# Optimization experiments

Measured on AMD Instinct MI355X. Metric: run time of the kernel, lower is better.

## Reference

```python
import jax, jax.numpy as jnp
import numpy as np

D_MODEL = 2048
NUM_EXPERTS = 128
TOP_K = 8
NORM_P = 2.0  # normalize_expert_weights


def setup_inputs() -> dict:
    key = jax.random.key(0)
    k1, k2 = jax.random.split(key)
    x = jax.random.normal(k1, (4, 4096, D_MODEL), dtype=jnp.float32)
    # router weight ~ trunc_normal(std=0.02); plain normal*0.02 is fine for a numeric baseline
    weight = jax.random.normal(k2, (NUM_EXPERTS, D_MODEL), dtype=jnp.float32) * 0.02
    score_bias = jnp.zeros((NUM_EXPERTS,), dtype=jnp.float32)
    return {"x": x, "weight": weight, "score_bias": score_bias}


def reference(x, weight, score_bias):
    # Flatten tokens: (B, S, D) -> (N, D); router always runs in fp32 (x.float())
    B, S, D = x.shape
    xf = x.reshape(B * S, D).astype(jnp.float32)
    # get_expert_logits: F.linear(x, weight.view(E, D)) -> (N, E)
    logits = jnp.einsum("nd,ed->ne", xf, weight.astype(jnp.float32))
    # softmax gating
    scores = jax.nn.softmax(logits, axis=-1)
    # bias-adjusted top-k (bias only affects selection, not the returned weights)
    biased = scores + score_bias[None, :]
    _, expert_indices = jax.lax.top_k(biased, TOP_K)          # (N, top_k)
    expert_weights = jnp.take_along_axis(scores, expert_indices, axis=-1)
    # normalize_expert_weights = 2.0 -> divide by L2 norm across top_k
    norm = jnp.linalg.norm(expert_weights, ord=NORM_P, axis=-1, keepdims=True)
    expert_weights = expert_weights / norm
    return expert_weights, expert_indices
```

## Files before the change

kernel.cpp:

```cpp
#include <hip/hip_runtime.h>
#include <math.h>


#define NE      128
#define TOKT    64
#define KC      32
#define DMODEL  2048
#define NT      (DMODEL / KC)
#define CHUNK_SH (3 * NE * KC)

typedef __attribute__((ext_vector_type(8))) short short8;
typedef __attribute__((ext_vector_type(4))) short s16x4;
typedef __attribute__((ext_vector_type(4))) float f32x4;

union S4u { short s[4]; s16x4 v; };

__device__ __forceinline__ void split3(float f, S4u& hi, S4u& mi, S4u& lo, int j) {
  const unsigned u0 = __float_as_uint(f);
  const float hif = __uint_as_float(u0 & 0xFFFF0000u);
  const float r1 = f - hif;
  const unsigned u1 = __float_as_uint(r1);
  const float mif = __uint_as_float(u1 & 0xFFFF0000u);
  const float r2 = r1 - mif;
  hi.s[j] = (short)(u0 >> 16);
  mi.s[j] = (short)(u1 >> 16);
  lo.s[j] = (short)(__float_as_uint(r2) >> 16);
}

__global__ __launch_bounds__(256) void wprep(const float* __restrict__ w,
                                             short* __restrict__ wp) {
  const int gid = blockIdx.x * 256 + threadIdx.x;
  const int e = gid >> 9;
  const int g = gid & 511;
  const int k = g << 2;
  const int chunk = k >> 5;
  const int kk = k & 31;
  const f32x4 a = *(const f32x4*)(w + (size_t)e * DMODEL + k);
  S4u hi, mi, lo;
  split3(a[0], hi, mi, lo, 0); split3(a[1], hi, mi, lo, 1);
  split3(a[2], hi, mi, lo, 2); split3(a[3], hi, mi, lo, 3);
  short* base = wp + (size_t)chunk * CHUNK_SH + (size_t)e * KC + kk;
  *(s16x4*)(base)               = hi.v;
  *(s16x4*)(base + NE * KC)     = mi.v;
  *(s16x4*)(base + 2 * NE * KC) = lo.v;
}

__device__ __forceinline__ void gll16(const short* g, short* l) {
  __builtin_amdgcn_global_load_lds(
      (const __attribute__((address_space(1))) void*)g,
      (__attribute__((address_space(3))) void*)l, 16, 0, 0);
}

__global__ __launch_bounds__(512) void router_fused(
    const float* __restrict__ x, const short* __restrict__ wp,
    const float* __restrict__ bias, float* __restrict__ outW,
    float* __restrict__ outI, int N) {
  __shared__ __align__(16) short xsm[2][3][TOKT][KC];
  __shared__ __align__(16) short wsm[2][3][NE][KC];
  __shared__ float L[TOKT][NE + 2];

  const int tid  = threadIdx.x;
  const int wv   = tid >> 6;
  const int lane = tid & 63;
  const int wm   = wv >> 2;
  const int wn   = wv & 3;
  const int quad = lane >> 4;
  const int l16  = lane & 15;
  const size_t tokBase = (size_t)blockIdx.x * TOKT;

  const int r  = tid >> 3;
  const int kq = tid & 7;
  const float* xg = x + (tokBase + r) * (size_t)DMODEL + kq * 4;

  f32x4 accs[4][2][2];
#pragma unroll
  for (int s = 0; s < 4; ++s)
#pragma unroll
    for (int i = 0; i < 2; ++i)
#pragma unroll
      for (int j = 0; j < 2; ++j) accs[s][i][j] = (f32x4)(0.f);

  auto stage_w = [&](int buf, int chunk) {
    const short* gsrc = wp + (size_t)chunk * CHUNK_SH + wv * 512 + lane * 8;
    short* ldst = &wsm[buf][0][0][0] + wv * 512;
    gll16(gsrc,        ldst);
    gll16(gsrc + 4096, ldst + 4096);
    gll16(gsrc + 8192, ldst + 8192);
  };
  auto stage_x = [&](int buf, f32x4 xr) {
    S4u hi, mi, lo;
    split3(xr[0], hi, mi, lo, 0); split3(xr[1], hi, mi, lo, 1);
    split3(xr[2], hi, mi, lo, 2); split3(xr[3], hi, mi, lo, 3);
    *(s16x4*)&xsm[buf][0][r][kq * 4] = hi.v;
    *(s16x4*)&xsm[buf][1][r][kq * 4] = mi.v;
    *(s16x4*)&xsm[buf][2][r][kq * 4] = lo.v;
  };
  auto compute = [&](int buf, f32x4 (&acc)[2][2]) {
    short8 af[2][3];
#pragma unroll
    for (int mt = 0; mt < 2; ++mt)
#pragma unroll
      for (int p = 0; p < 3; ++p)
        af[mt][p] = *(const short8*)&xsm[buf][p][wm * 32 + mt * 16 + l16][quad * 8];
#pragma unroll
    for (int nt = 0; nt < 2; ++nt) {
      short8 bf[3];
#pragma unroll
      for (int p = 0; p < 3; ++p)
        bf[p] = *(const short8*)&wsm[buf][p][wn * 32 + nt * 16 + l16][quad * 8];
#pragma unroll
      for (int mt = 0; mt < 2; ++mt) {
        f32x4 c = acc[mt][nt];
        c = __builtin_amdgcn_mfma_f32_16x16x32_bf16(af[mt][0], bf[0], c, 0, 0, 0);
        c = __builtin_amdgcn_mfma_f32_16x16x32_bf16(af[mt][0], bf[1], c, 0, 0, 0);
        c = __builtin_amdgcn_mfma_f32_16x16x32_bf16(af[mt][1], bf[0], c, 0, 0, 0);
        c = __builtin_amdgcn_mfma_f32_16x16x32_bf16(af[mt][0], bf[2], c, 0, 0, 0);
        c = __builtin_amdgcn_mfma_f32_16x16x32_bf16(af[mt][2], bf[0], c, 0, 0, 0);
        c = __builtin_amdgcn_mfma_f32_16x16x32_bf16(af[mt][1], bf[1], c, 0, 0, 0);
        acc[mt][nt] = c;
      }
    }
  };

  stage_w(0, 0);
  f32x4 xra = *(const f32x4*)(xg);
  f32x4 xrb = *(const f32x4*)(xg + KC);
  stage_x(0, xra);
  __syncthreads();

#pragma unroll
  for (int s = 0; s < 4; ++s) {
#pragma unroll 1
    for (int u = 0; u < 16; u += 2) {
      const int t = s * 16 + u;
      if (t + 1 < NT) stage_w(1, t + 1);
      if (t + 2 < NT) xra = *(const f32x4*)(xg + (t + 2) * KC);
      compute(0, accs[s]);
      if (t + 1 < NT) { stage_x(1, xrb); __syncthreads(); }
      if (t + 2 < NT) stage_w(0, t + 2);
      if (t + 3 < NT) xrb = *(const f32x4*)(xg + (t + 3) * KC);
      if (t + 1 < NT) compute(1, accs[s]);
      if (t + 2 < NT) { stage_x(0, xra); __syncthreads(); }
    }
  }

#pragma unroll
  for (int mt = 0; mt < 2; ++mt)
#pragma unroll
    for (int nt = 0; nt < 2; ++nt)
#pragma unroll
      for (int reg = 0; reg < 4; ++reg) {
        float v = accs[0][mt][nt][reg];
        v += accs[1][mt][nt][reg];
        v += accs[2][mt][nt][reg];
        v += accs[3][mt][nt][reg];
        L[wm * 32 + mt * 16 + quad * 4 + reg][wn * 32 + nt * 16 + l16] = v;
      }
  __syncthreads();

  const float bmy0 = bias[lane];
  const float bmy1 = bias[lane + 64];
  for (int i = 0; i < 8; ++i) {
    const int tk = wv * 8 + i;
    const float l0 = L[tk][lane];
    const float l1 = L[tk][lane + 64];

    float m = fmaxf(l0, l1);
#pragma unroll
    for (int off = 1; off < 64; off <<= 1) m = fmaxf(m, __shfl_xor(m, off));
    const float ev0 = __expf(l0 - m);
    const float ev1 = __expf(l1 - m);
    float zs = ev0 + ev1;
#pragma unroll
    for (int off = 1; off < 64; off <<= 1) zs += __shfl_xor(zs, off);
    const float s0 = ev0 / zs;
    const float s1 = ev1 / zs;

    float b0 = s0 + bmy0;
    float b1 = s1 + bmy1;

    float myv = 0.f;
    int myi = 0;
    float ss = 0.f;
#pragma unroll
    for (int rnd = 0; rnd < 8; ++rnd) {
      float key; int idx;
      if (b0 >= b1) { key = b0; idx = lane; }
      else          { key = b1; idx = lane + 64; }
#pragma unroll
      for (int off = 1; off < 64; off <<= 1) {
        const float k2 = __shfl_xor(key, off);
        const int   i2 = __shfl_xor(idx, off);
        if (k2 > key || (k2 == key && i2 < idx)) { key = k2; idx = i2; }
      }
      const float cand = (idx < 64) ? s0 : s1;
      const float sw = __shfl(cand, idx & 63);
      ss = fmaf(sw, sw, ss);
      if (lane == rnd) { myv = sw; myi = idx; }
      if (lane == (idx & 63)) { if (idx < 64) b0 = -INFINITY; else b1 = -INFINITY; }
    }

    const float inv = 1.f / sqrtf(ss);
    if (lane < 8) {
      const size_t tok = tokBase + tk;
      outW[tok * 8 + lane] = myv * inv;
      outI[tok * 8 + lane] = (float)myi;
    }
  }
}

extern "C" void kernel_launch(void* const* d_in, const int* in_sizes, int n_in,
                              void* d_out, int out_size, void* d_ws, size_t ws_size,
                              hipStream_t stream) {
  const float* x    = (const float*)d_in[0];
  const float* w    = (const float*)d_in[1];
  const float* bias = (const float*)d_in[2];
  float* out = (float*)d_out;

  const int N = in_sizes[0] / DMODEL;
  short* wp = (short*)d_ws;

  wprep<<<256, 256, 0, stream>>>(w, wp);
  router_fused<<<N / TOKT, 512, 0, stream>>>(x, wp, bias, out, out + (size_t)N * 8, N);
}
```

Before: 271.6 us.

## Load router weight fragments directly into registers instead of staging through LDS

```diff
diff --git a/kernel.cpp b/kernel.cpp
--- a/kernel.cpp
+++ b/kernel.cpp
@@ -8,6 +8,7 @@
 #define DMODEL  2048
 #define NT      (DMODEL / KC)
 #define CHUNK_SH (3 * NE * KC)
+#define XPAD    40
 
 typedef __attribute__((ext_vector_type(8))) short short8;
 typedef __attribute__((ext_vector_type(4))) short s16x4;
@@ -45,19 +46,14 @@
   *(s16x4*)(base + 2 * NE * KC) = lo.v;
 }
 
-__device__ __forceinline__ void gll16(const short* g, short* l) {
-  __builtin_amdgcn_global_load_lds(
-      (const __attribute__((address_space(1))) void*)g,
-      (__attribute__((address_space(3))) void*)l, 16, 0, 0);
-}
-
 __global__ __launch_bounds__(512) void router_fused(
     const float* __restrict__ x, const short* __restrict__ wp,
     const float* __restrict__ bias, float* __restrict__ outW,
     float* __restrict__ outI, int N) {
-  __shared__ __align__(16) short xsm[2][3][TOKT][KC];
-  __shared__ __align__(16) short wsm[2][3][NE][KC];
-  __shared__ float L[TOKT][NE + 2];
+  __shared__ __align__(16) char arena[TOKT * (NE + 2) * 4];
+  typedef short XsmT[3][TOKT][XPAD];
+  XsmT* xsm = (XsmT*)arena;
+  float (*L)[NE + 2] = (float (*)[NE + 2])arena;
 
   const int tid  = threadIdx.x;
   const int wv   = tid >> 6;
@@ -72,6 +68,8 @@
   const int kq = tid & 7;
   const float* xg = x + (tokBase + r) * (size_t)DMODEL + kq * 4;
 
+  const short* wfb = wp + (size_t)(wn * 32 + l16) * KC + quad * 8;
+
   f32x4 accs[4][2][2];
 #pragma unroll
   for (int s = 0; s < 4; ++s)
@@ -80,12 +78,13 @@
 #pragma unroll
       for (int j = 0; j < 2; ++j) accs[s][i][j] = (f32x4)(0.f);
 
-  auto stage_w = [&](int buf, int chunk) {
-    const short* gsrc = wp + (size_t)chunk * CHUNK_SH + wv * 512 + lane * 8;
-    short* ldst = &wsm[buf][0][0][0] + wv * 512;
-    gll16(gsrc,        ldst);
-    gll16(gsrc + 4096, ldst + 4096);
-    gll16(gsrc + 8192, ldst + 8192);
+  auto load_bf = [&](short8 (&bf)[2][3], int c) {
+    const short* b = wfb + (size_t)c * CHUNK_SH;
+#pragma unroll
+    for (int nt = 0; nt < 2; ++nt)
+#pragma unroll
+      for (int p = 0; p < 3; ++p)
+        bf[nt][p] = *(const short8*)(b + p * (NE * KC) + nt * 16 * KC);
   };
   auto stage_x = [&](int buf, f32x4 xr) {
     S4u hi, mi, lo;
@@ -95,7 +94,7 @@
     *(s16x4*)&xsm[buf][1][r][kq * 4] = mi.v;
     *(s16x4*)&xsm[buf][2][r][kq * 4] = lo.v;
   };
-  auto compute = [&](int buf, f32x4 (&acc)[2][2]) {
+  auto compute = [&](int buf, const short8 (&bf)[2][3], f32x4 (&acc)[2][2]) {
     short8 af[2][3];
 #pragma unroll
     for (int mt = 0; mt < 2; ++mt)
@@ -103,46 +102,48 @@
       for (int p = 0; p < 3; ++p)
         af[mt][p] = *(const short8*)&xsm[buf][p][wm * 32 + mt * 16 + l16][quad * 8];
 #pragma unroll
-    for (int nt = 0; nt < 2; ++nt) {
-      short8 bf[3];
-#pragma unroll
-      for (int p = 0; p < 3; ++p)
-        bf[p] = *(const short8*)&wsm[buf][p][wn * 32 + nt * 16 + l16][quad * 8];
+    for (int nt = 0; nt < 2; ++nt)
 #pragma unroll
       for (int mt = 0; mt < 2; ++mt) {
         f32x4 c = acc[mt][nt];
-        c = __builtin_amdgcn_mfma_f32_16x16x32_bf16(af[mt][0], bf[0], c, 0, 0, 0);
-        c = __builtin_amdgcn_mfma_f32_16x16x32_bf16(af[mt][0], bf[1], c, 0, 0, 0);
-        c = __builtin_amdgcn_mfma_f32_16x16x32_bf16(af[mt][1], bf[0], c, 0, 0, 0);
-        c = __builtin_amdgcn_mfma_f32_16x16x32_bf16(af[mt][0], bf[2], c, 0, 0, 0);
-        c = __builtin_amdgcn_mfma_f32_16x16x32_bf16(af[mt][2], bf[0], c, 0, 0, 0);
-        c = __builtin_amdgcn_mfma_f32_16x16x32_bf16(af[mt][1], bf[1], c, 0, 0, 0);
+        c = __builtin_amdgcn_mfma_f32_16x16x32_bf16(af[mt][0], bf[nt][0], c, 0, 0, 0);
+        c = __builtin_amdgcn_mfma_f32_16x16x32_bf16(af[mt][0], bf[nt][1], c, 0, 0, 0);
+        c = __builtin_amdgcn_mfma_f32_16x16x32_bf16(af[mt][1], bf[nt][0], c, 0, 0, 0);
+        c = __builtin_amdgcn_mfma_f32_16x16x32_bf16(af[mt][0], bf[nt][2], c, 0, 0, 0);
+        c = __builtin_amdgcn_mfma_f32_16x16x32_bf16(af[mt][2], bf[nt][0], c, 0, 0, 0);
+        c = __builtin_amdgcn_mfma_f32_16x16x32_bf16(af[mt][1], bf[nt][1], c, 0, 0, 0);
         acc[mt][nt] = c;
       }
-    }
-  };
-
-  stage_w(0, 0);
+  };
+  auto lds_barrier = [&]() {
+    asm volatile("s_waitcnt lgkmcnt(0)" ::: "memory");
+    __builtin_amdgcn_s_barrier();
+  };
+
+  short8 bfA[2][3], bfB[2][3];
+  load_bf(bfA, 0);
   f32x4 xra = *(const f32x4*)(xg);
   f32x4 xrb = *(const f32x4*)(xg + KC);
   stage_x(0, xra);
-  __syncthreads();
+  lds_barrier();
 
 #pragma unroll
   for (int s = 0; s < 4; ++s) {
 #pragma unroll 1
     for (int u = 0; u < 16; u += 2) {
       const int t = s * 16 + u;
-      if (t + 1 < NT) stage_w(1, t + 1);
+      if (t + 1 < NT) load_bf(bfB, t + 1);
       if (t + 2 < NT) xra = *(const f32x4*)(xg + (t + 2) * KC);
-      compute(0, accs[s]);
-      if (t + 1 < NT) { stage_x(1, xrb); __syncthreads(); }
-      if (t + 2 < NT) stage_w(0, t + 2);
+      compute(0, bfA, accs[s]);
+      if (t + 1 < NT) { stage_x(1, xrb); lds_barrier(); }
+      if (t + 2 < NT) load_bf(bfA, t + 2);
       if (t + 3 < NT) xrb = *(const f32x4*)(xg + (t + 3) * KC);
-      if (t + 1 < NT) compute(1, accs[s]);
-      if (t + 2 < NT) { stage_x(0, xra); __syncthreads(); }
+      if (t + 1 < NT) compute(1, bfB, accs[s]);
+      if (t + 2 < NT) { stage_x(0, xra); lds_barrier(); }
     }
   }
+
+  __syncthreads();
 
 #pragma unroll
   for (int mt = 0; mt < 2; ++mt)
```

Result: no change. 273.6 us (+0.7%).

## Drop LDS staging: load operands directly to registers with split-K across waves

Applied to the files above, without the earlier changes.

```diff
diff --git a/kernel.cpp b/kernel.cpp
--- a/kernel.cpp
+++ b/kernel.cpp
@@ -3,7 +3,7 @@
 
 
 #define NE      128
-#define TOKT    64
+#define TOKT    32
 #define KC      32
 #define DMODEL  2048
 #define NT      (DMODEL / KC)
@@ -13,9 +13,22 @@
 typedef __attribute__((ext_vector_type(4))) short s16x4;
 typedef __attribute__((ext_vector_type(4))) float f32x4;
 
+union S8  { short s[8]; short8 v; };
 union S4u { short s[4]; s16x4 v; };
 
-__device__ __forceinline__ void split3(float f, S4u& hi, S4u& mi, S4u& lo, int j) {
+__device__ __forceinline__ void split3(float f, S8& hi, S8& mi, S8& lo, int j) {
+  const unsigned u0 = __float_as_uint(f);
+  const float hif = __uint_as_float(u0 & 0xFFFF0000u);
+  const float r1 = f - hif;
+  const unsigned u1 = __float_as_uint(r1);
+  const float mif = __uint_as_float(u1 & 0xFFFF0000u);
+  const float r2 = r1 - mif;
+  hi.s[j] = (short)(u0 >> 16);
+  mi.s[j] = (short)(u1 >> 16);
+  lo.s[j] = (short)(__float_as_uint(r2) >> 16);
+}
+
+__device__ __forceinline__ void split3w(float f, S4u& hi, S4u& mi, S4u& lo, int j) {
   const unsigned u0 = __float_as_uint(f);
   const float hif = __uint_as_float(u0 & 0xFFFF0000u);
   const float r1 = f - hif;
@@ -37,133 +50,114 @@
   const int kk = k & 31;
   const f32x4 a = *(const f32x4*)(w + (size_t)e * DMODEL + k);
   S4u hi, mi, lo;
-  split3(a[0], hi, mi, lo, 0); split3(a[1], hi, mi, lo, 1);
-  split3(a[2], hi, mi, lo, 2); split3(a[3], hi, mi, lo, 3);
+  split3w(a[0], hi, mi, lo, 0); split3w(a[1], hi, mi, lo, 1);
+  split3w(a[2], hi, mi, lo, 2); split3w(a[3], hi, mi, lo, 3);
   short* base = wp + (size_t)chunk * CHUNK_SH + (size_t)e * KC + kk;
   *(s16x4*)(base)               = hi.v;
   *(s16x4*)(base + NE * KC)     = mi.v;
   *(s16x4*)(base + 2 * NE * KC) = lo.v;
 }
 
-__device__ __forceinline__ void gll16(const short* g, short* l) {
-  __builtin_amdgcn_global_load_lds(
-      (const __attribute__((address_space(1))) void*)g,
-      (__attribute__((address_space(3))) void*)l, 16, 0, 0);
-}
-
-__global__ __launch_bounds__(512) void router_fused(
+__global__ __launch_bounds__(512, 4) void router_fused(
     const float* __restrict__ x, const short* __restrict__ wp,
     const float* __restrict__ bias, float* __restrict__ outW,
     float* __restrict__ outI, int N) {
-  __shared__ __align__(16) short xsm[2][3][TOKT][KC];
-  __shared__ __align__(16) short wsm[2][3][NE][KC];
-  __shared__ float L[TOKT][NE + 2];
+  __shared__ float Lp[4][TOKT][NE + 2];
 
   const int tid  = threadIdx.x;
   const int wv   = tid >> 6;
   const int lane = tid & 63;
-  const int wm   = wv >> 2;
-  const int wn   = wv & 3;
+  const int sl   = wv >> 1;
+  const int h    = wv & 1;
   const int quad = lane >> 4;
   const int l16  = lane & 15;
   const size_t tokBase = (size_t)blockIdx.x * TOKT;
 
-  const int r  = tid >> 3;
-  const int kq = tid & 7;
-  const float* xg = x + (tokBase + r) * (size_t)DMODEL + kq * 4;
-
-  f32x4 accs[4][2][2];
-#pragma unroll
-  for (int s = 0; s < 4; ++s)
-#pragma unroll
-    for (int i = 0; i < 2; ++i)
-#pragma unroll
-      for (int j = 0; j < 2; ++j) accs[s][i][j] = (f32x4)(0.f);
-
-  auto stage_w = [&](int buf, int chunk) {
-    const short* gsrc = wp + (size_t)chunk * CHUNK_SH + wv * 512 + lane * 8;
-    short* ldst = &wsm[buf][0][0][0] + wv * 512;
-    gll16(gsrc,        ldst);
-    gll16(gsrc + 4096, ldst + 4096);
-    gll16(gsrc + 8192, ldst + 8192);
+  const float* xg = x + (tokBase + l16) * (size_t)DMODEL + quad * 8;
+  const short* wfb = wp + (size_t)(h * 64 + l16) * KC + quad * 8;
+
+  f32x4 acc[2][4];
+#pragma unroll
+  for (int mt = 0; mt < 2; ++mt)
+#pragma unroll
+    for (int nt = 0; nt < 4; ++nt) acc[mt][nt] = (f32x4)(0.f);
+
+  short8 bfbuf[2][3];
+  auto load_bf = [&](int b, int t, int nt) {
+    const short* p0 = wfb + (size_t)t * CHUNK_SH + nt * (16 * KC);
+#pragma unroll
+    for (int p = 0; p < 3; ++p)
+      bfbuf[b][p] = *(const short8*)(p0 + p * (NE * KC));
   };
-  auto stage_x = [&](int buf, f32x4 xr) {
-    S4u hi, mi, lo;
-    split3(xr[0], hi, mi, lo, 0); split3(xr[1], hi, mi, lo, 1);
-    split3(xr[2], hi, mi, lo, 2); split3(xr[3], hi, mi, lo, 3);
-    *(s16x4*)&xsm[buf][0][r][kq * 4] = hi.v;
-    *(s16x4*)&xsm[buf][1][r][kq * 4] = mi.v;
-    *(s16x4*)&xsm[buf][2][r][kq * 4] = lo.v;
-  };
-  auto compute = [&](int buf, f32x4 (&acc)[2][2]) {
+
+  load_bf(0, sl * 16, 0);
+#pragma unroll 1
+  for (int u = 0; u < 16; ++u) {
+    const int t = sl * 16 + u;
+    const float* xp0 = xg + (size_t)t * KC;
+    const float* xp1 = xp0 + 16 * (size_t)DMODEL;
+    const f32x4 x0a = *(const f32x4*)(xp0);
+    const f32x4 x0b = *(const f32x4*)(xp0 + 4);
+    const f32x4 x1a = *(const f32x4*)(xp1);
+    const f32x4 x1b = *(const f32x4*)(xp1 + 4);
     short8 af[2][3];
-#pragma unroll
-    for (int mt = 0; mt < 2; ++mt)
-#pragma unroll
-      for (int p = 0; p < 3; ++p)
-        af[mt][p] = *(const short8*)&xsm[buf][p][wm * 32 + mt * 16 + l16][quad * 8];
-#pragma unroll
-    for (int nt = 0; nt < 2; ++nt) {
-      short8 bf[3];
-#pragma unroll
-      for (int p = 0; p < 3; ++p)
-        bf[p] = *(const short8*)&wsm[buf][p][wn * 32 + nt * 16 + l16][quad * 8];
+    {
+      S8 hi, mi, lo;
+      split3(x0a[0], hi, mi, lo, 0); split3(x0a[1], hi, mi, lo, 1);
+      split3(x0a[2], hi, mi, lo, 2); split3(x0a[3], hi, mi, lo, 3);
+      split3(x0b[0], hi, mi, lo, 4); split3(x0b[1], hi, mi, lo, 5);
+      split3(x0b[2], hi, mi, lo, 6); split3(x0b[3], hi, mi, lo, 7);
+      af[0][0] = hi.v; af[0][1] = mi.v; af[0][2] = lo.v;
+    }
+    {
+      S8 hi, mi, lo;
+      split3(x1a[0], hi, mi, lo, 0); split3(x1a[1], hi, mi, lo, 1);
+      split3(x1a[2], hi, mi, lo, 2); split3(x1a[3], hi, mi, lo, 3);
+      split3(x1b[0], hi, mi, lo, 4); split3(x1b[1], hi, mi, lo, 5);
+      split3(x1b[2], hi, mi, lo, 6); split3(x1b[3], hi, mi, lo, 7);
+      af[1][0] = hi.v; af[1][1] = mi.v; af[1][2] = lo.v;
+    }
+#pragma unroll
+    for (int nt = 0; nt < 4; ++nt) {
+      if (nt < 3)           load_bf((nt + 1) & 1, t, nt + 1);
+      else if (u + 1 < 16)  load_bf(0, t + 1, 0);
+      const int b = nt & 1;
 #pragma unroll
       for (int mt = 0; mt < 2; ++mt) {
         f32x4 c = acc[mt][nt];
-        c = __builtin_amdgcn_mfma_f32_16x16x32_bf16(af[mt][0], bf[0], c, 0, 0, 0);
-        c = __builtin_amdgcn_mfma_f32_16x16x32_bf16(af[mt][0], bf[1], c, 0, 0, 0);
-        c = __builtin_amdgcn_mfma_f32_16x16x32_bf16(af[mt][1], bf[0], c, 0, 0, 0);
-        c = __builtin_amdgcn_mfma_f32_16x16x32_bf16(af[mt][0], bf[2], c, 0, 0, 0);
-        c = __builtin_amdgcn_mfma_f32_16x16x32_bf16(af[mt][2], bf[0], c, 0, 0, 0);
-        c = __builtin_amdgcn_mfma_f32_16x16x32_bf16(af[mt][1], bf[1], c, 0, 0, 0);
+        c = __builtin_amdgcn_mfma_f32_16x16x32_bf16(af[mt][0], bfbuf[b][0], c, 0, 0, 0);
+        c = __builtin_amdgcn_mfma_f32_16x16x32_bf16(af[mt][0], bfbuf[b][1], c, 0, 0, 0);
+        c = __builtin_amdgcn_mfma_f32_16x16x32_bf16(af[mt][1], bfbuf[b][0], c, 0, 0, 0);
+        c = __builtin_amdgcn_mfma_f32_16x16x32_bf16(af[mt][0], bfbuf[b][2], c, 0, 0, 0);
+        c = __builtin_amdgcn_mfma_f32_16x16x32_bf16(af[mt][2], bfbuf[b][0], c, 0, 0, 0);
+        c = __builtin_amdgcn_mfma_f32_16x16x32_bf16(af[mt][1], bfbuf[b][1], c, 0, 0, 0);
         acc[mt][nt] = c;
       }
     }
-  };
-
-  stage_w(0, 0);
-  f32x4 xra = *(const f32x4*)(xg);
-  f32x4 xrb = *(const f32x4*)(xg + KC);
-  stage_x(0, xra);
-  __syncthreads();
-
-#pragma unroll
-  for (int s = 0; s < 4; ++s) {
-#pragma unroll 1
-    for (int u = 0; u < 16; u += 2) {
-      const int t = s * 16 + u;
-      if (t + 1 < NT) stage_w(1, t + 1);
-      if (t + 2 < NT) xra = *(const f32x4*)(xg + (t + 2) * KC);
-      compute(0, accs[s]);
-      if (t + 1 < NT) { stage_x(1, xrb); __syncthreads(); }
-      if (t + 2 < NT) stage_w(0, t + 2);
-      if (t + 3 < NT) xrb = *(const f32x4*)(xg + (t + 3) * KC);
-      if (t + 1 < NT) compute(1, accs[s]);
-      if (t + 2 < NT) { stage_x(0, xra); __syncthreads(); }
-    }
   }
 
 #pragma unroll
   for (int mt = 0; mt < 2; ++mt)
 #pragma unroll
-    for (int nt = 0; nt < 2; ++nt)
-#pragma unroll
-      for (int reg = 0; reg < 4; ++reg) {
-        float v = accs[0][mt][nt][reg];
-        v += accs[1][mt][nt][reg];
-        v += accs[2][mt][nt][reg];
-        v += accs[3][mt][nt][reg];
-        L[wm * 32 + mt * 16 + quad * 4 + reg][wn * 32 + nt * 16 + l16] = v;
-      }
+    for (int nt = 0; nt < 4; ++nt)
+#pragma unroll
+      for (int reg = 0; reg < 4; ++reg)
+        Lp[sl][mt * 16 + quad * 4 + reg][h * 64 + nt * 16 + l16] =
+            acc[mt][nt][reg];
   __syncthreads();
 
   const float bmy0 = bias[lane];
   const float bmy1 = bias[lane + 64];
-  for (int i = 0; i < 8; ++i) {
-    const int tk = wv * 8 + i;
-    const float l0 = L[tk][lane];
-    const float l1 = L[tk][lane + 64];
+  for (int i = 0; i < 4; ++i) {
+    const int tk = wv * 4 + i;
+    float l0 = Lp[0][tk][lane];
+    l0 += Lp[1][tk][lane];
+    l0 += Lp[2][tk][lane];
+    l0 += Lp[3][tk][lane];
+    float l1 = Lp[0][tk][lane + 64];
+    l1 += Lp[1][tk][lane + 64];
+    l1 += Lp[2][tk][lane + 64];
+    l1 += Lp[3][tk][lane + 64];
 
     float m = fmaxf(l0, l1);
 #pragma unroll
```

New measurement: 260.3 us. 1.04x faster.
